# Kernel tuning notes

Hardware: AMD Instinct MI355X
Metric: run time of the kernel (lower is better)

Reference implementation:

```python
import jax, jax.numpy as jnp
import numpy as np

H = 1024       # hidden_size
E = 1024       # embedding_size
V = 50257      # output_size (vocab)
L = 64         # max_length


def setup_inputs() -> dict:
    key = jax.random.key(0)
    ks = jax.random.split(key, 12)
    s = 0.02
    return {
        "input": jax.random.randint(ks[0], (1,), 0, V),
        "hidden": jax.random.normal(ks[1], (1, 1, H), dtype=jnp.float32),
        "encoder_outputs": jax.random.normal(ks[2], (L, H), dtype=jnp.float32),
        "emb": jax.random.normal(ks[3], (V, E), dtype=jnp.float32) * s,
        "attn_w": jax.random.normal(ks[4], (L, H + E), dtype=jnp.float32) * s,
        "attn_b": jnp.zeros((L,), dtype=jnp.float32),
        "comb_w": jax.random.normal(ks[5], (E, H + E), dtype=jnp.float32) * s,
        "comb_b": jnp.zeros((E,), dtype=jnp.float32),
        "w_ih": jax.random.normal(ks[6], (3 * H, E), dtype=jnp.float32) * s,
        "b_ih": jnp.zeros((3 * H,), dtype=jnp.float32),
        "w_hh": jax.random.normal(ks[7], (3 * H, H), dtype=jnp.float32) * s,
        "b_hh": jnp.zeros((3 * H,), dtype=jnp.float32),
        "out_w": jax.random.normal(ks[8], (V, H), dtype=jnp.float32) * s,
        "out_b": jnp.zeros((V,), dtype=jnp.float32),
    }


def reference(input, hidden, encoder_outputs, emb, attn_w, attn_b,
              comb_w, comb_b, w_ih, b_ih, w_hh, b_hh, out_w, out_b):
    # embedding + (dropout = identity in eval)
    embedded = emb[input].reshape(1, E)            # [1, E]
    h0 = hidden[0]                                  # [1, H]
    # Bahdanau-style attention over fixed-length encoder outputs
    attn_logits = jnp.concatenate([embedded, h0], axis=1) @ attn_w.T + attn_b
    attn_weights = jax.nn.softmax(attn_logits, axis=1)      # [1, L]
    attn_applied = attn_weights @ encoder_outputs            # [1, H]
    x = jnp.concatenate([embedded, attn_applied], axis=1) @ comb_w.T + comb_b
    x = jax.nn.relu(x)                               # [1, E]
    # single GRU cell step (torch gate order: r, z, n)
    gi = x @ w_ih.T + b_ih
    gh = h0 @ w_hh.T + b_hh
    i_r, i_z, i_n = jnp.split(gi, 3, axis=1)
    h_r, h_z, h_n = jnp.split(gh, 3, axis=1)
    r = jax.nn.sigmoid(i_r + h_r)
    z = jax.nn.sigmoid(i_z + h_z)
    n = jnp.tanh(i_n + r * h_n)
    h_new = (1.0 - z) * n + z * h0                   # [1, H]
    logp = jax.nn.log_softmax(h_new @ out_w.T + out_b, axis=1)  # [1, V]
    return logp, h_new[None], attn_weights
```

## Files before the change

kernel.cpp:

```cpp
#include <hip/hip_runtime.h>
#include <math.h>

#define H 1024
#define E 1024
#define V 50257
#define L 64
#define HE 2048

__device__ inline float dot4(float4 a, float4 b) {
    return a.x*b.x + a.y*b.y + a.z*b.z + a.w*b.w;
}

__device__ inline float wave_reduce_sum(float v) {
    #pragma unroll
    for (int off = 32; off > 0; off >>= 1)
        v += __shfl_down(v, off, 64);
    return v;
}

__global__ __launch_bounds__(512) void k_front(
        const int* __restrict__ inp,
        const float* __restrict__ hidden,
        const float* __restrict__ enc,
        const float* __restrict__ emb,
        const float* __restrict__ attn_w,
        const float* __restrict__ attn_b,
        const float* __restrict__ comb_w,
        const float* __restrict__ comb_b,
        float* __restrict__ x,
        float* __restrict__ out_weights) {
    const int bid  = blockIdx.x;
    const int t    = threadIdx.x;
    const int wave = t >> 6;
    const int lane = t & 63;

    __shared__ float lgS[L];
    __shared__ float sig[L];
    __shared__ __align__(16) float aa[H];

    const float* erow = emb + (size_t)inp[0] * E;
    const float4* e4 = (const float4*)erow;
    const float4* h4 = (const float4*)hidden;

    float4 ev[4], hv[4];
    #pragma unroll
    for (int i = 0; i < 4; ++i) { ev[i] = e4[i * 64 + lane]; hv[i] = h4[i * 64 + lane]; }

    float s[8];
    #pragma unroll
    for (int r = 0; r < 8; ++r) {
        int row = wave * 8 + r;
        const float4* w = (const float4*)(attn_w + (size_t)row * HE);
        float acc = 0.f;
        #pragma unroll
        for (int i = 0; i < 4; ++i) acc += dot4(w[i * 64 + lane], ev[i]);
        #pragma unroll
        for (int i = 0; i < 4; ++i) acc += dot4(w[256 + i * 64 + lane], hv[i]);
        s[r] = acc;
    }
    #pragma unroll
    for (int r = 0; r < 8; ++r) s[r] = wave_reduce_sum(s[r]);
    if (lane == 0) {
        #pragma unroll
        for (int r = 0; r < 8; ++r) {
            int row = wave * 8 + r;
            lgS[row] = s[r] + attn_b[row];
        }
    }
    __syncthreads();
    if (t < 64) {
        float v = lgS[t];
        float m = v;
        #pragma unroll
        for (int off = 32; off > 0; off >>= 1) m = fmaxf(m, __shfl_xor(m, off, 64));
        float ex = expf(v - m);
        float ssum = ex;
        #pragma unroll
        for (int off = 32; off > 0; off >>= 1) ssum += __shfl_xor(ssum, off, 64);
        float w = ex / ssum;
        sig[t] = w;
        if (bid == 0) out_weights[t] = w;
    }
    __syncthreads();
    {
        float a0 = 0.f, a1 = 0.f;
        #pragma unroll 8
        for (int l = 0; l < L; ++l) {
            float sl = sig[l];
            a0 += sl * enc[l * H + t];
            a1 += sl * enc[l * H + t + 512];
        }
        aa[t] = a0;
        aa[t + 512] = a1;
    }
    __syncthreads();
    {
        int row = bid * 8 + wave;
        const float4* wr = (const float4*)(comb_w + (size_t)row * HE);
        const float4* a4 = (const float4*)aa;
        float acc = 0.f;
        #pragma unroll
        for (int i = 0; i < 4; ++i) acc += dot4(wr[i * 64 + lane], ev[i]);
        #pragma unroll
        for (int i = 0; i < 4; ++i) acc += dot4(wr[256 + i * 64 + lane], a4[i * 64 + lane]);
        acc = wave_reduce_sum(acc);
        if (lane == 0) x[row] = fmaxf(acc + comb_b[row], 0.f);
    }
}

__global__ __launch_bounds__(768) void k_gru(
        const float* __restrict__ x,
        const float* __restrict__ hidden,
        const float* __restrict__ w_ih,
        const float* __restrict__ b_ih,
        const float* __restrict__ w_hh,
        const float* __restrict__ b_hh,
        float* __restrict__ h_new) {
    int t = threadIdx.x, wave = t >> 6, lane = t & 63;
    int g  = wave >> 2;
    int j4 = wave & 3;
    int j  = blockIdx.x * 4 + j4;
    const float4* x4 = (const float4*)x;
    const float4* h4 = (const float4*)hidden;
    const float4* wi = (const float4*)(w_ih + (size_t)(g * H + j) * E);
    const float4* wh = (const float4*)(w_hh + (size_t)(g * H + j) * H);
    float si = 0.f, sh = 0.f;
    #pragma unroll
    for (int i = 0; i < 4; ++i) {
        int idx = i * 64 + lane;
        si += dot4(wi[idx], x4[idx]);
        sh += dot4(wh[idx], h4[idx]);
    }
    #pragma unroll
    for (int off = 32; off > 0; off >>= 1) {
        si += __shfl_down(si, off, 64);
        sh += __shfl_down(sh, off, 64);
    }
    __shared__ float redI[3][4], redH[3][4];
    if (lane == 0) {
        redI[g][j4] = si + b_ih[g * H + j];
        redH[g][j4] = sh + b_hh[g * H + j];
    }
    __syncthreads();
    if (t < 4) {
        int jo = blockIdx.x * 4 + t;
        float i_r = redI[0][t], i_z = redI[1][t], i_n = redI[2][t];
        float h_r = redH[0][t], h_z = redH[1][t], h_n = redH[2][t];
        float r = 1.f / (1.f + expf(-(i_r + h_r)));
        float z = 1.f / (1.f + expf(-(i_z + h_z)));
        float n = tanhf(i_n + r * h_n);
        h_new[jo] = (1.f - z) * n + z * hidden[jo];
    }
}

__global__ __launch_bounds__(256) void k_vocab(
        const float* __restrict__ h_new,
        const float* __restrict__ out_w,
        const float* __restrict__ out_b,
        float* __restrict__ logp,
        float* __restrict__ partials) {
    int t = threadIdx.x, wave = t >> 6, lane = t & 63;
    const float4* h4 = (const float4*)h_new;
    float4 hv[4];
    #pragma unroll
    for (int i = 0; i < 4; ++i) hv[i] = h4[i * 64 + lane];
    int base = blockIdx.x * 16 + wave * 4;
    float s[4] = {0.f, 0.f, 0.f, 0.f};
    if (base + 3 < V) {
        const float4* w0 = (const float4*)(out_w + (size_t)(base + 0) * H);
        const float4* w1 = (const float4*)(out_w + (size_t)(base + 1) * H);
        const float4* w2 = (const float4*)(out_w + (size_t)(base + 2) * H);
        const float4* w3 = (const float4*)(out_w + (size_t)(base + 3) * H);
        #pragma unroll
        for (int i = 0; i < 4; ++i) {
            int idx = i * 64 + lane;
            s[0] += dot4(w0[idx], hv[i]);
            s[1] += dot4(w1[idx], hv[i]);
            s[2] += dot4(w2[idx], hv[i]);
            s[3] += dot4(w3[idx], hv[i]);
        }
    } else {
        #pragma unroll
        for (int k = 0; k < 4; ++k)
            if (base + k < V) {
                const float4* w = (const float4*)(out_w + (size_t)(base + k) * H);
                #pragma unroll
                for (int i = 0; i < 4; ++i) s[k] += dot4(w[i * 64 + lane], hv[i]);
            }
    }
    #pragma unroll
    for (int off = 32; off > 0; off >>= 1) {
        s[0] += __shfl_down(s[0], off, 64);
        s[1] += __shfl_down(s[1], off, 64);
        s[2] += __shfl_down(s[2], off, 64);
        s[3] += __shfl_down(s[3], off, 64);
    }
    __shared__ float smP[4];
    if (lane == 0) {
        float pe = 0.f;
        #pragma unroll
        for (int k = 0; k < 4; ++k) {
            int r = base + k;
            if (r < V) {
                float v = s[k] + out_b[r];
                logp[r] = v;
                pe += expf(v);
            }
        }
        smP[wave] = pe;
    }
    __syncthreads();
    if (t == 0)
        partials[blockIdx.x] = smP[0] + smP[1] + smP[2] + smP[3];
}

__global__ __launch_bounds__(256) void k_lsm(
        float* __restrict__ logp,
        const float* __restrict__ partials, int nb) {
    int t = threadIdx.x;
    float S = 0.f;
    for (int i = t; i < nb; i += 256) S += partials[i];
    S = wave_reduce_sum(S);
    __shared__ float ss[4];
    __shared__ float sh_lz;
    if ((t & 63) == 0) ss[t >> 6] = S;
    __syncthreads();
    if (t == 0) sh_lz = logf(ss[0] + ss[1] + ss[2] + ss[3]);
    __syncthreads();
    float lz = sh_lz;
    int i = blockIdx.x * 256 + t;
    if (i < V) logp[i] -= lz;
}

extern "C" void kernel_launch(void* const* d_in, const int* in_sizes, int n_in,
                              void* d_out, int out_size, void* d_ws, size_t ws_size,
                              hipStream_t stream) {
    const int*   inp     = (const int*)d_in[0];
    const float* hidden  = (const float*)d_in[1];
    const float* enc     = (const float*)d_in[2];
    const float* emb     = (const float*)d_in[3];
    const float* attn_w  = (const float*)d_in[4];
    const float* attn_b  = (const float*)d_in[5];
    const float* comb_w  = (const float*)d_in[6];
    const float* comb_b  = (const float*)d_in[7];
    const float* w_ih    = (const float*)d_in[8];
    const float* b_ih    = (const float*)d_in[9];
    const float* w_hh    = (const float*)d_in[10];
    const float* b_hh    = (const float*)d_in[11];
    const float* out_w   = (const float*)d_in[12];
    const float* out_b   = (const float*)d_in[13];

    float* out          = (float*)d_out;
    float* logp         = out;
    float* h_new        = out + V;
    float* attn_weights = out + V + H;

    float* ws       = (float*)d_ws;
    float* x        = ws;
    float* partials = ws + 1024;
    const int nb = (V + 15) / 16;

    k_front<<<128, 512, 0, stream>>>(inp, hidden, enc, emb, attn_w, attn_b,
                                     comb_w, comb_b, x, attn_weights);
    k_gru<<<256, 768, 0, stream>>>(x, hidden, w_ih, b_ih, w_hh, b_hh, h_new);
    k_vocab<<<nb, 256, 0, stream>>>(h_new, out_w, out_b, logp, partials);
    k_lsm<<<(V + 255) / 256, 256, 0, stream>>>(logp, partials, nb);
}
```

Measured before the change: 70.13 us.

## Split attention logits into separate kernel to avoid redundant per-block computation

The front kernel previously recomputed all 64 attention logits in every one of its 128 blocks, reading the full attn_w matrix (512 KB) each time. That work now runs in a new kernel with one block per logit row, which writes the logits to workspace, and the combine kernel reads them back. This removes redundant weight reads and arithmetic but adds one kernel launch and a global-memory round trip on the critical path.

```diff
diff --git a/kernel.cpp b/kernel.cpp
--- a/kernel.cpp
+++ b/kernel.cpp
@@ -18,13 +18,34 @@
     return v;
 }
 
-__global__ __launch_bounds__(512) void k_front(
+__global__ __launch_bounds__(256) void k_lg(
+        const int* __restrict__ inp,
+        const float* __restrict__ hidden,
+        const float* __restrict__ emb,
+        const float* __restrict__ attn_w,
+        const float* __restrict__ attn_b,
+        float* __restrict__ lg) {
+    const int b = blockIdx.x;
+    const int t = threadIdx.x;
+    const int wave = t >> 6, lane = t & 63;
+    const float* erow = emb + (size_t)inp[0] * E;
+    const float4* e4 = (const float4*)erow;
+    const float4* h4 = (const float4*)hidden;
+    const float4* w  = (const float4*)(attn_w + (size_t)b * HE);
+    float s = dot4(w[t], e4[t]) + dot4(w[256 + t], h4[t]);
+    s = wave_reduce_sum(s);
+    __shared__ float red[4];
+    if (lane == 0) red[wave] = s;
+    __syncthreads();
+    if (t == 0) lg[b] = red[0] + red[1] + red[2] + red[3] + attn_b[b];
+}
+
+__global__ __launch_bounds__(512) void k_comb(
         const int* __restrict__ inp,
         const float* __restrict__ hidden,
         const float* __restrict__ enc,
         const float* __restrict__ emb,
-        const float* __restrict__ attn_w,
-        const float* __restrict__ attn_b,
+        const float* __restrict__ lg,
         const float* __restrict__ comb_w,
         const float* __restrict__ comb_b,
         float* __restrict__ x,
@@ -34,42 +55,14 @@
     const int wave = t >> 6;
     const int lane = t & 63;
 
-    __shared__ float lgS[L];
     __shared__ float sig[L];
     __shared__ __align__(16) float aa[H];
 
     const float* erow = emb + (size_t)inp[0] * E;
     const float4* e4 = (const float4*)erow;
-    const float4* h4 = (const float4*)hidden;
-
-    float4 ev[4], hv[4];
-    #pragma unroll
-    for (int i = 0; i < 4; ++i) { ev[i] = e4[i * 64 + lane]; hv[i] = h4[i * 64 + lane]; }
-
-    float s[8];
-    #pragma unroll
-    for (int r = 0; r < 8; ++r) {
-        int row = wave * 8 + r;
-        const float4* w = (const float4*)(attn_w + (size_t)row * HE);
-        float acc = 0.f;
-        #pragma unroll
-        for (int i = 0; i < 4; ++i) acc += dot4(w[i * 64 + lane], ev[i]);
-        #pragma unroll
-        for (int i = 0; i < 4; ++i) acc += dot4(w[256 + i * 64 + lane], hv[i]);
-        s[r] = acc;
-    }
-    #pragma unroll
-    for (int r = 0; r < 8; ++r) s[r] = wave_reduce_sum(s[r]);
-    if (lane == 0) {
-        #pragma unroll
-        for (int r = 0; r < 8; ++r) {
-            int row = wave * 8 + r;
-            lgS[row] = s[r] + attn_b[row];
-        }
-    }
-    __syncthreads();
+
     if (t < 64) {
-        float v = lgS[t];
+        float v = lg[t];
         float m = v;
         #pragma unroll
         for (int off = 32; off > 0; off >>= 1) m = fmaxf(m, __shfl_xor(m, off, 64));
@@ -100,7 +93,7 @@
         const float4* a4 = (const float4*)aa;
         float acc = 0.f;
         #pragma unroll
-        for (int i = 0; i < 4; ++i) acc += dot4(wr[i * 64 + lane], ev[i]);
+        for (int i = 0; i < 4; ++i) acc += dot4(wr[i * 64 + lane], e4[i * 64 + lane]);
         #pragma unroll
         for (int i = 0; i < 4; ++i) acc += dot4(wr[256 + i * 64 + lane], a4[i * 64 + lane]);
         acc = wave_reduce_sum(acc);
@@ -256,12 +249,14 @@
     float* attn_weights = out + V + H;
 
     float* ws       = (float*)d_ws;
-    float* x        = ws;
-    float* partials = ws + 1024;
+    float* lg       = ws;
+    float* x        = ws + 64;
+    float* partials = ws + 1088;
     const int nb = (V + 15) / 16;
 
-    k_front<<<128, 512, 0, stream>>>(inp, hidden, enc, emb, attn_w, attn_b,
-                                     comb_w, comb_b, x, attn_weights);
+    k_lg<<<64, 256, 0, stream>>>(inp, hidden, emb, attn_w, attn_b, lg);
+    k_comb<<<128, 512, 0, stream>>>(inp, hidden, enc, emb, lg,
+                                    comb_w, comb_b, x, attn_weights);
     k_gru<<<256, 768, 0, stream>>>(x, hidden, w_ih, b_ih, w_hh, b_hh, h_new);
     k_vocab<<<nb, 256, 0, stream>>>(h_new, out_w, out_b, logp, partials);
     k_lsm<<<(V + 255) / 256, 256, 0, stream>>>(logp, partials, nb);
```

New measurement: 66.67 us. 1.05x faster.
